# Kernel optimization log

Hardware: AMD Instinct MI355X
Metric: run time of the kernel (lower is better)

Reference implementation:

```python
import jax, jax.numpy as jnp
import numpy as np

D_MODEL = 512
D_STATE = 16
D_CONV = 4
EXPAND = 2
D_INNER = EXPAND * D_MODEL  # 1024
DT_RANK = D_MODEL // 16     # 32 (ceil(512/16))
BATCH, SEQ = 8, 1024


def setup_inputs() -> dict:
    key = jax.random.key(0)
    ks = jax.random.split(key, 10)
    w = lambda i, shape, s=0.02: (jax.random.normal(ks[i], shape, jnp.float32) * s)
    return {
        "x": jax.random.normal(ks[0], (BATCH, SEQ, D_MODEL), jnp.float32),
        # Mamba params
        "W_in": w(1, (2 * D_INNER, D_MODEL)),            # in_proj (no bias)
        "conv_w": w(2, (D_INNER, D_CONV), 0.1),          # depthwise causal conv
        "conv_b": jnp.zeros((D_INNER,), jnp.float32),
        "W_x": w(3, (DT_RANK + 2 * D_STATE, D_INNER)),   # x_proj (no bias)
        "W_dt": w(4, (D_INNER, DT_RANK)),                # dt_proj
        "b_dt": jnp.full((D_INNER,), -4.6, jnp.float32), # -> softplus ~ 0.01
        "A_log": jnp.log(jnp.broadcast_to(
            jnp.arange(1, D_STATE + 1, dtype=jnp.float32), (D_INNER, D_STATE))),
        "D": jnp.ones((D_INNER,), jnp.float32),
        "W_out": w(5, (D_MODEL, D_INNER)),               # out_proj (no bias)
        # LayerNorm + head
        "ln_g": jnp.ones((D_MODEL,), jnp.float32),
        "ln_b": jnp.zeros((D_MODEL,), jnp.float32),
        "head_W": w(6, (D_MODEL, D_MODEL)),
        "head_b": jnp.zeros((D_MODEL,), jnp.float32),
    }


def reference(x, W_in, conv_w, conv_b, W_x, W_dt, b_dt, A_log, D, W_out,
              ln_g, ln_b, head_W, head_b):
    B, L, _ = x.shape
    # in_proj -> split into x branch and gate z
    xz = x @ W_in.T                               # (B, L, 2*D_INNER)
    xi, z = jnp.split(xz, 2, axis=-1)
    # causal depthwise conv1d over time (pad left d_conv-1), then SiLU
    xp = jnp.pad(xi, ((0, 0), (D_CONV - 1, 0), (0, 0)))
    xc = conv_b + sum(conv_w[:, k] * xp[:, k:k + L, :] for k in range(D_CONV))
    xc = jax.nn.silu(xc)                          # (B, L, D_INNER)
    # x_proj -> dt, B, C
    dbc = xc @ W_x.T
    dt = jax.nn.softplus(dbc[..., :DT_RANK] @ W_dt.T + b_dt)   # (B, L, D_INNER)
    Bm = dbc[..., DT_RANK:DT_RANK + D_STATE]                   # (B, L, D_STATE)
    Cm = dbc[..., DT_RANK + D_STATE:]                          # (B, L, D_STATE)
    A = -jnp.exp(A_log)                                        # (D_INNER, D_STATE)

    def step(h, ins):
        dt_t, B_t, C_t, u_t = ins                 # (B,Din) (B,Ds) (B,Ds) (B,Din)
        dA = jnp.exp(dt_t[:, :, None] * A)        # (B, Din, Ds)
        h = dA * h + (dt_t * u_t)[:, :, None] * B_t[:, None, :]
        y = jnp.einsum('bds,bs->bd', h, C_t)
        return h, y

    h0 = jnp.zeros((B, D_INNER, D_STATE), x.dtype)
    xs = (dt.transpose(1, 0, 2), Bm.transpose(1, 0, 2),
          Cm.transpose(1, 0, 2), xc.transpose(1, 0, 2))
    _, ys = jax.lax.scan(step, h0, xs)            # ys: (L, B, D_INNER)
    y = ys.transpose(1, 0, 2) + D * xc
    y = y * jax.nn.silu(z)
    out = y @ W_out.T                             # (B, L, D_MODEL)
    # LayerNorm is per-token, so norm the last token only (== LN(out)[:, -1])
    last = out[:, -1, :]
    mu = last.mean(-1, keepdims=True)
    var = ((last - mu) ** 2).mean(-1, keepdims=True)
    lastn = (last - mu) / jnp.sqrt(var + 1e-5) * ln_g + ln_b
    return lastn @ head_W.T + head_b              # (B, D_MODEL)
```

## Files before the change

kernel.cpp:

```cpp
#include <hip/hip_runtime.h>
#include <stdint.h>

#define B_   8
#define L_   1024
#define DM   512
#define DI   1024
#define DS   16
#define DTR  32
#define M_   (B_*L_)

typedef short v8s __attribute__((ext_vector_type(8)));
typedef short v4s __attribute__((ext_vector_type(4)));
typedef float v4f __attribute__((ext_vector_type(4)));

static __device__ __forceinline__ short f2bf(float f) {
  union { float f; uint32_t u; } v; v.f = f;
  uint32_t r = v.u + 0x7FFFu + ((v.u >> 16) & 1u);
  return (short)(r >> 16);
}
static __device__ __forceinline__ float bf2f(short s) {
  union { uint32_t u; float f; } v; v.u = ((uint32_t)(uint16_t)s) << 16; return v.f;
}
static __device__ __forceinline__ float silu_fast(float a) {
  return a * __builtin_amdgcn_rcpf(1.f + __expf(-a));
}
static __device__ __forceinline__ float wsum(float v) {
#pragma unroll
  for (int o = 32; o > 0; o >>= 1) v += __shfl_xor(v, o, 64);
  return v;
}
static __device__ __forceinline__ void gl_lds16(const short* g, short* l) {
  __builtin_amdgcn_global_load_lds(
      (const __attribute__((address_space(1))) void*)g,
      (__attribute__((address_space(3))) void*)l, 16, 0, 0);
}

__global__ __launch_bounds__(256) void k_prep(const float* __restrict__ x,
                                              const float* __restrict__ w_in,
                                              const float* __restrict__ w_x,
                                              const float* __restrict__ w_dt,
                                              const float* __restrict__ a_log,
                                              short* xb, short* wib, short* wxb, short* wdtb,
                                              float* Aneg, float* zlast) {
  if (blockIdx.x >= 4704) {
    int w = (int)(blockIdx.x - 4704) * 4 + (threadIdx.x >> 6);
    int l = threadIdx.x & 63;
    int b = w >> 10, j = w & 1023;
    const v4f* xr = (const v4f*)(x + ((size_t)(b * L_ + L_ - 1)) * DM);
    const v4f* wr = (const v4f*)(w_in + (size_t)(DI + j) * DM);
    float s = 0.f;
#pragma unroll
    for (int i = 0; i < 2; ++i) {
      v4f a = xr[l + 64 * i], c = wr[l + 64 * i];
      s += a[0]*c[0] + a[1]*c[1] + a[2]*c[2] + a[3]*c[3];
    }
    s = wsum(s);
    if (l == 0) zlast[b * DI + j] = s;
    return;
  }
  int idx = (blockIdx.x * 256 + threadIdx.x) * 4;
  const int n0 = M_ * DM, n1 = DI * DM, n2 = 48 * DI, n3 = DI * DTR, n4 = DI * DS;
  const float* src; short* dst;
  if (idx < n0)              { src = x + idx;    dst = xb + idx; }
  else if ((idx -= n0) < n1) { src = w_in + idx; dst = wib + idx; }
  else if ((idx -= n1) < n2) { src = w_x + idx;  dst = wxb + idx; }
  else if ((idx -= n2) < n3) { src = w_dt + idx; dst = wdtb + idx; }
  else if ((idx -= n3) < n4) {
    v4f v = *(const v4f*)(a_log + idx);
    v4f o;
#pragma unroll
    for (int i = 0; i < 4; ++i) o[i] = -__expf(v[i]);
    *(v4f*)(Aneg + idx) = o;
    return;
  }
  else return;
  v4f v = *(const v4f*)src;
  v4s o;
#pragma unroll
  for (int i = 0; i < 4; ++i) o[i] = f2bf(v[i]);
  *(v4s*)dst = o;
}

__global__ __launch_bounds__(256) void k_gemm_xi(const short* __restrict__ xb,
                                                 const short* __restrict__ wib,
                                                 short* __restrict__ xib) {
  __shared__ short sh[128 * 136];
  short* lA = sh;
  short* lB = sh + 128 * 64;
  int mb = blockIdx.x >> 3, nb = blockIdx.x & 7;
  int tid = threadIdx.x;
  int w = tid >> 6, l = tid & 63, lm = l & 15, q = l >> 4;
  int wm = (w >> 1) * 64, wn = (w & 1) * 64;

  v4f acc[4][4];
#pragma unroll
  for (int i = 0; i < 4; ++i)
#pragma unroll
    for (int j = 0; j < 4; ++j) acc[i][j] = (v4f){0,0,0,0};

  int srow_in_chunk = l >> 3;
  int sslot = l & 7;
  const short* Abase = xb  + (size_t)(mb * 128) * DM;
  const short* Bbase = wib + (size_t)(nb * 128) * DM;

  for (int k0 = 0; k0 < DM; k0 += 64) {
    if (k0) __syncthreads();
#pragma unroll
    for (int i = 0; i < 4; ++i) {
      int chunk = w * 4 + i;
      int row = chunk * 8 + srow_in_chunk;
      int c = sslot ^ (row & 7);
      gl_lds16(Abase + (size_t)row * DM + k0 + c * 8, lA + chunk * 512);
      gl_lds16(Bbase + (size_t)row * DM + k0 + c * 8, lB + chunk * 512);
    }
    __syncthreads();
#pragma unroll
    for (int kt = 0; kt < 2; ++kt) {
      v8s af[4], bf[4];
      int p = (kt * 4 + q) ^ (lm & 7);
#pragma unroll
      for (int t = 0; t < 4; ++t) {
        af[t] = *(const v8s*)(lA + (wm + t * 16 + lm) * 64 + p * 8);
        bf[t] = *(const v8s*)(lB + (wn + t * 16 + lm) * 64 + p * 8);
      }
#pragma unroll
      for (int i = 0; i < 4; ++i)
#pragma unroll
        for (int j = 0; j < 4; ++j)
          acc[i][j] = __builtin_amdgcn_mfma_f32_16x16x32_bf16(af[i], bf[j], acc[i][j], 0, 0, 0);
    }
  }
  __syncthreads();
#pragma unroll
  for (int i = 0; i < 4; ++i)
#pragma unroll
    for (int r = 0; r < 4; ++r) {
      int row = wm + i * 16 + q * 4 + r;
#pragma unroll
      for (int j = 0; j < 4; ++j)
        sh[row * 136 + wn + j * 16 + lm] = f2bf(acc[i][j][r]);
    }
  __syncthreads();
  int cc = tid & 15;
#pragma unroll
  for (int g = 0; g < 8; ++g) {
    int rr = (tid >> 4) + g * 16;
    v8s v = *(const v8s*)(sh + rr * 136 + cc * 8);
    *(v8s*)(xib + (size_t)(mb * 128 + rr) * DI + nb * 128 + cc * 8) = v;
  }
}

__global__ __launch_bounds__(256) void k_conv(const short* __restrict__ xib,
                                              const float* __restrict__ conv_w,
                                              const float* __restrict__ conv_b,
                                              short* __restrict__ xcb,
                                              float* __restrict__ xclast) {
  int bid = blockIdx.x;
  int b = bid >> 7, tc = bid & 127;
  int tid = threadIdx.x;
  int d8 = tid & 127, th = tid >> 7;
  int d = d8 * 8;
  int t0 = tc * 8 + th * 4;
  v4f cw[8];
  float cb[8];
#pragma unroll
  for (int i = 0; i < 8; ++i) {
    cw[i] = *(const v4f*)(conv_w + (d + i) * 4);
    cb[i] = conv_b[d + i];
  }
  float w0[8], w1[8], w2[8];
  const short* base = xib + (size_t)(b * L_) * DI + d;
  short* obase = xcb + (size_t)(b * L_) * DI + d;
#pragma unroll
  for (int i = 0; i < 8; ++i) { w0[i] = 0.f; w1[i] = 0.f; w2[i] = 0.f; }
  if (t0 >= 3) {
    v8s v0 = *(const v8s*)(base + (size_t)(t0 - 3) * DI);
    v8s v1 = *(const v8s*)(base + (size_t)(t0 - 2) * DI);
    v8s v2 = *(const v8s*)(base + (size_t)(t0 - 1) * DI);
#pragma unroll
    for (int i = 0; i < 8; ++i) { w0[i] = bf2f(v0[i]); w1[i] = bf2f(v1[i]); w2[i] = bf2f(v2[i]); }
  }
#pragma unroll
  for (int t = t0; t < t0 + 4; ++t) {
    v8s cur = *(const v8s*)(base + (size_t)t * DI);
    v8s ob;
#pragma unroll
    for (int i = 0; i < 8; ++i) {
      float xv = bf2f(cur[i]);
      float a = cb[i] + cw[i][0] * w0[i] + cw[i][1] * w1[i] + cw[i][2] * w2[i] + cw[i][3] * xv;
      float s = silu_fast(a);
      ob[i] = f2bf(s);
      if (t == L_ - 1) xclast[b * DI + d + i] = s;
      w0[i] = w1[i]; w1[i] = w2[i]; w2[i] = xv;
    }
    *(v8s*)(obase + (size_t)t * DI) = ob;
  }
}

__global__ __launch_bounds__(256) void k_dbcdt(const short* __restrict__ xcb,
                                               const short* __restrict__ wxb,
                                               const short* __restrict__ wdtb,
                                               const float* __restrict__ b_dt,
                                               float* __restrict__ Bmat,
                                               _Float16* __restrict__ dtO,
                                               float* __restrict__ csum2) {
  __shared__ union {
    float red[4 * 16 * 49];
    _Float16 dtile[16 * 1024];
  } u;
  __shared__ short ta[16 * 32];
  int m = blockIdx.x;
  int tid = threadIdx.x, w = tid >> 6, l = tid & 63, lm = l & 15, q = l >> 4;
  v4f a0 = {0,0,0,0}, a1 = {0,0,0,0}, a2 = {0,0,0,0};
  const short* ap = xcb + (size_t)(m * 16 + lm) * DI + w * 256 + q * 8;
  const short* b0 = wxb + (size_t)lm * DI        + w * 256 + q * 8;
  const short* b1 = wxb + (size_t)(16 + lm) * DI + w * 256 + q * 8;
  const short* b2 = wxb + (size_t)(32 + lm) * DI + w * 256 + q * 8;
#pragma unroll
  for (int kk = 0; kk < 8; ++kk) {
    v8s a = *(const v8s*)(ap + kk * 32);
    a0 = __builtin_amdgcn_mfma_f32_16x16x32_bf16(a, *(const v8s*)(b0 + kk * 32), a0, 0, 0, 0);
    a1 = __builtin_amdgcn_mfma_f32_16x16x32_bf16(a, *(const v8s*)(b1 + kk * 32), a1, 0, 0, 0);
    a2 = __builtin_amdgcn_mfma_f32_16x16x32_bf16(a, *(const v8s*)(b2 + kk * 32), a2, 0, 0, 0);
  }
#pragma unroll
  for (int r = 0; r < 4; ++r) {
    int row = q * 4 + r;
    u.red[w * 784 + row * 49 + lm]      = a0[r];
    u.red[w * 784 + row * 49 + 16 + lm] = a1[r];
    u.red[w * 784 + row * 49 + 32 + lm] = a2[r];
  }
  __syncthreads();
  {
    int row = tid >> 4, c0 = tid & 15;
    int base = row * 49 + c0;
    float s0 = u.red[base] + u.red[784 + base] + u.red[1568 + base] + u.red[2352 + base];
    float s1 = u.red[base + 16] + u.red[784 + base + 16] + u.red[1568 + base + 16] + u.red[2352 + base + 16];
    float s2 = u.red[base + 32] + u.red[784 + base + 32] + u.red[1568 + base + 32] + u.red[2352 + base + 32];
    ta[row * 32 + c0]      = f2bf(s0);
    ta[row * 32 + 16 + c0] = f2bf(s1);
    Bmat[(size_t)(m * 16 + row) * DS + c0] = s2;
  }
  __syncthreads();
  v8s ad = *(const v8s*)(ta + lm * 32 + q * 8);
#pragma unroll 4
  for (int nn = 0; nn < 16; ++nn) {
    int nt = w * 16 + nn;
    v8s bb = *(const v8s*)(wdtb + (size_t)(nt * 16 + lm) * DTR + q * 8);
    v4f zz = {0,0,0,0};
    v4f dd = __builtin_amdgcn_mfma_f32_16x16x32_bf16(ad, bb, zz, 0, 0, 0);
    int col = nt * 16 + lm;
    float bd = b_dt[col];
    float s = 0.f;
#pragma unroll
    for (int r = 0; r < 4; ++r) {
      float v = dd[r] + bd;
      float sp = (v > 15.f) ? v : __logf(1.f + __expf(v));
      u.dtile[(q * 4 + r) * 1024 + col] = (_Float16)sp;
      s += sp;
    }
    s += __shfl_xor(s, 16, 64);
    s += __shfl_xor(s, 32, 64);
    if (q == 0) csum2[(size_t)m * DI + col] = s;
  }
  __syncthreads();
#pragma unroll
  for (int row = 0; row < 16; ++row) {
    v4s v = *(const v4s*)(u.dtile + row * 1024 + tid * 4);
    *(v4s*)(dtO + (size_t)(m * 16 + row) * DI + tid * 4) = v;
  }
}

__global__ __launch_bounds__(256) void k_sufc(const float* __restrict__ csum2,
                                              const float* __restrict__ xclast,
                                              const float* __restrict__ w_x,
                                              float* __restrict__ SS,
                                              float* __restrict__ clast) {
  if (blockIdx.x < 32) {
    int b = blockIdx.x >> 2, dseg = blockIdx.x & 3;
    int d = dseg * 256 + threadIdx.x;
    float run = 0.f;
    for (int ch = 31; ch >= 0; --ch) {
      SS[(size_t)(b * 32 + ch) * DI + d] = run;
      run += csum2[(size_t)(b * 64 + 2 * ch + 1) * DI + d]
           + csum2[(size_t)(b * 64 + 2 * ch) * DI + d];
    }
  } else {
    int w2 = (int)(blockIdx.x - 32) * 4 + (threadIdx.x >> 6);
    int l = threadIdx.x & 63;
    int b = w2 >> 4, ss = w2 & 15;
    const v4f* xr = (const v4f*)(xclast + (size_t)b * DI);
    const v4f* wr = (const v4f*)(w_x + (size_t)(48 + ss) * DI);
    float s = 0.f;
#pragma unroll
    for (int i = 0; i < 4; ++i) {
      v4f a = xr[l + 64 * i], c = wr[l + 64 * i];
      s += a[0]*c[0] + a[1]*c[1] + a[2]*c[2] + a[3]*c[3];
    }
    s = wsum(s);
    if (l == 0) clast[b * 16 + ss] = s;
  }
}

__global__ __launch_bounds__(256) void k_scan(const _Float16* __restrict__ dt,
                                              const short* __restrict__ xcb,
                                              const float* __restrict__ Bmat,
                                              const float* __restrict__ SS,
                                              const float* __restrict__ Aneg,
                                              const float* __restrict__ clast,
                                              float* __restrict__ ypart) {
  __shared__ float lB[32 * 16];
  int bid = blockIdx.x;
  int b = bid >> 7, ch = (bid >> 2) & 31, dg = bid & 3;
  int tid = threadIdx.x;
  for (int i = tid; i < 32 * 16; i += 256)
    lB[i] = Bmat[(size_t)(b * L_ + ch * 32) * DS + i];
  __syncthreads();
  int d = dg * 256 + tid;
  float S = SS[(size_t)(b * 32 + ch) * DI + d];
  float As2[16];
#pragma unroll
  for (int s = 0; s < 16; ++s) As2[s] = Aneg[d * 16 + s] * 1.44269504f;
  float h[16];
#pragma unroll
  for (int s = 0; s < 16; ++s) h[s] = 0.f;
  const _Float16* dtp = dt + ((size_t)(b * L_ + ch * 32)) * DI + d;
  const short* xcp = xcb + ((size_t)(b * L_ + ch * 32)) * DI + d;
  for (int tl = 31; tl >= 0; --tl) {
    float dtv = (float)dtp[(size_t)tl * DI];
    float u   = bf2f(xcp[(size_t)tl * DI]);
    float c = dtv * u;
#pragma unroll
    for (int s = 0; s < 16; ++s)
      h[s] += __builtin_amdgcn_exp2f(As2[s] * S) * (c * lB[tl * 16 + s]);
    S += dtv;
  }
  float yp = 0.f;
#pragma unroll
  for (int s = 0; s < 16; ++s) yp += h[s] * clast[b * 16 + s];
  ypart[(size_t)(b * 32 + ch) * DI + d] = yp;
}

__global__ __launch_bounds__(256) void k_ylast(const float* __restrict__ ypart,
                                               const float* __restrict__ xclast,
                                               const float* __restrict__ Dp,
                                               const float* __restrict__ zlast,
                                               float* __restrict__ ylast) {
  int idx = blockIdx.x * 256 + threadIdx.x;
  int b = idx >> 10, d = idx & 1023;
  float acc = 0.f;
#pragma unroll 8
  for (int ch = 0; ch < 32; ++ch) acc += ypart[(size_t)(b * 32 + ch) * DI + d];
  float y = acc + Dp[d] * xclast[idx];
  ylast[idx] = y * silu_fast(zlast[idx]);
}

__global__ __launch_bounds__(256) void k_out(const float* __restrict__ ylast,
                                             const float* __restrict__ w_out,
                                             float* __restrict__ olast) {
  int w = blockIdx.x * 4 + (threadIdx.x >> 6);
  int l = threadIdx.x & 63;
  int b = w >> 9, i = w & 511;
  const v4f* yr = (const v4f*)(ylast + (size_t)b * DI);
  const v4f* wr = (const v4f*)(w_out + (size_t)i * DI);
  float s = 0.f;
#pragma unroll
  for (int k = 0; k < 4; ++k) {
    v4f a = yr[l + 64 * k], c = wr[l + 64 * k];
    s += a[0]*c[0] + a[1]*c[1] + a[2]*c[2] + a[3]*c[3];
  }
  s = wsum(s);
  if (l == 0) olast[b * DM + i] = s;
}

__global__ __launch_bounds__(256) void k_ln(const float* __restrict__ olast,
                                            const float* __restrict__ g,
                                            const float* __restrict__ be,
                                            float* __restrict__ lastn) {
  __shared__ float s1[256], s2[256];
  int b = blockIdx.x, tid = threadIdx.x;
  float v0 = olast[b * DM + tid], v1 = olast[b * DM + 256 + tid];
  s1[tid] = v0 + v1; s2[tid] = v0 * v0 + v1 * v1;
  __syncthreads();
  for (int o = 128; o > 0; o >>= 1) {
    if (tid < o) { s1[tid] += s1[tid + o]; s2[tid] += s2[tid + o]; }
    __syncthreads();
  }
  float mu = s1[0] / (float)DM;
  float var = s2[0] / (float)DM - mu * mu;
  float inv = 1.f / sqrtf(var + 1e-5f);
  lastn[b * DM + tid]       = (v0 - mu) * inv * g[tid]       + be[tid];
  lastn[b * DM + 256 + tid] = (v1 - mu) * inv * g[tid + 256] + be[tid + 256];
}

__global__ __launch_bounds__(256) void k_head(const float* __restrict__ lastn,
                                              const float* __restrict__ hw,
                                              const float* __restrict__ hb,
                                              float* __restrict__ out) {
  int w = blockIdx.x * 4 + (threadIdx.x >> 6);
  int l = threadIdx.x & 63;
  int b = w >> 9, o = w & 511;
  const v4f* xr = (const v4f*)(lastn + (size_t)b * DM);
  const v4f* wr = (const v4f*)(hw + (size_t)o * DM);
  float s = 0.f;
#pragma unroll
  for (int k = 0; k < 2; ++k) {
    v4f a = xr[l + 64 * k], c = wr[l + 64 * k];
    s += a[0]*c[0] + a[1]*c[1] + a[2]*c[2] + a[3]*c[3];
  }
  s = wsum(s);
  if (l == 0) out[b * DM + o] = s + hb[o];
}

extern "C" void kernel_launch(void* const* d_in, const int* in_sizes, int n_in,
                              void* d_out, int out_size, void* d_ws, size_t ws_size,
                              hipStream_t stream) {
  const float* x      = (const float*)d_in[0];
  const float* w_in   = (const float*)d_in[1];
  const float* conv_w = (const float*)d_in[2];
  const float* conv_b = (const float*)d_in[3];
  const float* w_x    = (const float*)d_in[4];
  const float* w_dt   = (const float*)d_in[5];
  const float* b_dt   = (const float*)d_in[6];
  const float* a_log  = (const float*)d_in[7];
  const float* Dp     = (const float*)d_in[8];
  const float* w_out  = (const float*)d_in[9];
  const float* ln_g   = (const float*)d_in[10];
  const float* ln_b   = (const float*)d_in[11];
  const float* head_W = (const float*)d_in[12];
  const float* head_b = (const float*)d_in[13];
  float* out = (float*)d_out;

  char* ws = (char*)d_ws;
  size_t off = 0;
  auto alloc = [&](size_t bytes) { void* p = ws + off; off += (bytes + 255) & ~(size_t)255; return p; };
  short* xb     = (short*)alloc((size_t)M_*DM*2);
  short* wib    = (short*)alloc((size_t)DI*DM*2);
  short* wxb    = (short*)alloc((size_t)48*DI*2);
  short* wdtb   = (short*)alloc((size_t)DI*DTR*2);
  float* Aneg   = (float*)alloc((size_t)DI*DS*4);
  short* xib    = (short*)alloc((size_t)M_*DI*2);
  short* xcb    = (short*)alloc((size_t)M_*DI*2);
  _Float16* dt  = (_Float16*)alloc((size_t)M_*DI*2);
  float* Bmat   = (float*)alloc((size_t)M_*DS*4);
  float* csum2  = (float*)alloc((size_t)512*DI*4);
  float* SS     = (float*)alloc((size_t)B_*32*DI*4);
  float* ypart  = (float*)alloc((size_t)B_*32*DI*4);
  float* zlast  = (float*)alloc((size_t)B_*DI*4);
  float* clast  = (float*)alloc((size_t)B_*DS*4);
  float* xclast = (float*)alloc((size_t)B_*DI*4);
  float* ylast  = (float*)alloc((size_t)B_*DI*4);
  float* olast  = (float*)alloc((size_t)B_*DM*4);
  float* lastn  = (float*)alloc((size_t)B_*DM*4);

  k_prep<<<6752, 256, 0, stream>>>(x, w_in, w_x, w_dt, a_log, xb, wib, wxb, wdtb, Aneg, zlast);
  k_gemm_xi<<<512, 256, 0, stream>>>(xb, wib, xib);
  k_conv<<<1024, 256, 0, stream>>>(xib, conv_w, conv_b, xcb, xclast);
  k_dbcdt<<<512, 256, 0, stream>>>(xcb, wxb, wdtb, b_dt, Bmat, dt, csum2);
  k_sufc<<<64, 256, 0, stream>>>(csum2, xclast, w_x, SS, clast);
  k_scan<<<1024, 256, 0, stream>>>(dt, xcb, Bmat, SS, Aneg, clast, ypart);
  k_ylast<<<32, 256, 0, stream>>>(ypart, xclast, Dp, zlast, ylast);
  k_out<<<1024, 256, 0, stream>>>(ylast, w_out, olast);
  k_ln<<<8, 256, 0, stream>>>(olast, ln_g, ln_b, lastn);
  k_head<<<1024, 256, 0, stream>>>(lastn, head_W, head_b, out);
}
```

Measured before the change: 180.2 us.

## Fuse causal depthwise conv and SiLU into the in_proj GEMM epilogue

```diff
diff --git a/kernel.cpp b/kernel.cpp
--- a/kernel.cpp
+++ b/kernel.cpp
@@ -81,10 +81,14 @@
   *(v4s*)dst = o;
 }
 
-__global__ __launch_bounds__(256) void k_gemm_xi(const short* __restrict__ xb,
-                                                 const short* __restrict__ wib,
-                                                 short* __restrict__ xib) {
+__global__ __launch_bounds__(256) void k_gemm_xi_conv(const short* __restrict__ xb,
+                                                      const short* __restrict__ wib,
+                                                      const float* __restrict__ conv_w,
+                                                      const float* __restrict__ conv_b,
+                                                      short* __restrict__ xcb,
+                                                      float* __restrict__ xclast) {
   __shared__ short sh[128 * 136];
+  __shared__ short hs[3 * 128];
   short* lA = sh;
   short* lB = sh + 128 * 64;
   int mb = blockIdx.x >> 3, nb = blockIdx.x & 7;
@@ -140,60 +144,66 @@
       for (int j = 0; j < 4; ++j)
         sh[row * 136 + wn + j * 16 + lm] = f2bf(acc[i][j][r]);
     }
-  __syncthreads();
-  int cc = tid & 15;
-#pragma unroll
-  for (int g = 0; g < 8; ++g) {
-    int rr = (tid >> 4) + g * 16;
-    v8s v = *(const v8s*)(sh + rr * 136 + cc * 8);
-    *(v8s*)(xib + (size_t)(mb * 128 + rr) * DI + nb * 128 + cc * 8) = v;
-  }
-}
-
-__global__ __launch_bounds__(256) void k_conv(const short* __restrict__ xib,
-                                              const float* __restrict__ conv_w,
-                                              const float* __restrict__ conv_b,
-                                              short* __restrict__ xcb,
-                                              float* __restrict__ xclast) {
-  int bid = blockIdx.x;
-  int b = bid >> 7, tc = bid & 127;
-  int tid = threadIdx.x;
-  int d8 = tid & 127, th = tid >> 7;
-  int d = d8 * 8;
-  int t0 = tc * 8 + th * 4;
-  v4f cw[8];
-  float cb[8];
-#pragma unroll
-  for (int i = 0; i < 8; ++i) {
-    cw[i] = *(const v4f*)(conv_w + (d + i) * 4);
-    cb[i] = conv_b[d + i];
-  }
-  float w0[8], w1[8], w2[8];
-  const short* base = xib + (size_t)(b * L_) * DI + d;
-  short* obase = xcb + (size_t)(b * L_) * DI + d;
-#pragma unroll
-  for (int i = 0; i < 8; ++i) { w0[i] = 0.f; w1[i] = 0.f; w2[i] = 0.f; }
-  if (t0 >= 3) {
-    v8s v0 = *(const v8s*)(base + (size_t)(t0 - 3) * DI);
-    v8s v1 = *(const v8s*)(base + (size_t)(t0 - 2) * DI);
-    v8s v2 = *(const v8s*)(base + (size_t)(t0 - 1) * DI);
-#pragma unroll
-    for (int i = 0; i < 8; ++i) { w0[i] = bf2f(v0[i]); w1[i] = bf2f(v1[i]); w2[i] = bf2f(v2[i]); }
-  }
-#pragma unroll
-  for (int t = t0; t < t0 + 4; ++t) {
-    v8s cur = *(const v8s*)(base + (size_t)t * DI);
-    v8s ob;
-#pragma unroll
-    for (int i = 0; i < 8; ++i) {
-      float xv = bf2f(cur[i]);
-      float a = cb[i] + cw[i][0] * w0[i] + cw[i][1] * w1[i] + cw[i][2] * w2[i] + cw[i][3] * xv;
+  {
+    int t0 = (mb & 7) * 128;
+    int c = tid & 127;
+    if (t0 == 0) {
+      if (tid < 128) { hs[c] = 0; hs[128 + c] = 0; }
+      else           { hs[256 + c] = 0; }
+    } else {
+      const short* wrow = wib + (size_t)(nb * 128 + c) * DM;
+      if (tid < 128) {
+        const short* a0p = xb + (size_t)(mb * 128 - 3) * DM;
+        const short* a1p = xb + (size_t)(mb * 128 - 2) * DM;
+        float s0 = 0.f, s1 = 0.f;
+        for (int k = 0; k < DM; k += 8) {
+          v8s wv  = *(const v8s*)(wrow + k);
+          v8s av0 = *(const v8s*)(a0p + k);
+          v8s av1 = *(const v8s*)(a1p + k);
+#pragma unroll
+          for (int i = 0; i < 8; ++i) {
+            float wf = bf2f(wv[i]);
+            s0 += bf2f(av0[i]) * wf;
+            s1 += bf2f(av1[i]) * wf;
+          }
+        }
+        hs[c] = f2bf(s0); hs[128 + c] = f2bf(s1);
+      } else {
+        const short* a2p = xb + (size_t)(mb * 128 - 1) * DM;
+        float s2 = 0.f;
+        for (int k = 0; k < DM; k += 8) {
+          v8s wv  = *(const v8s*)(wrow + k);
+          v8s av2 = *(const v8s*)(a2p + k);
+#pragma unroll
+          for (int i = 0; i < 8; ++i) s2 += bf2f(av2[i]) * bf2f(wv[i]);
+        }
+        hs[256 + c] = f2bf(s2);
+      }
+    }
+  }
+  __syncthreads();
+  {
+    int c = tid & 127, th = tid >> 7;
+    int gcol = nb * 128 + c;
+    v4f cw = *(const v4f*)(conv_w + gcol * 4);
+    float cb = conv_b[gcol];
+    float w0, w1, w2;
+    if (th == 0) {
+      w0 = bf2f(hs[c]); w1 = bf2f(hs[128 + c]); w2 = bf2f(hs[256 + c]);
+    } else {
+      w0 = bf2f(sh[61 * 136 + c]); w1 = bf2f(sh[62 * 136 + c]); w2 = bf2f(sh[63 * 136 + c]);
+    }
+    size_t outbase = (size_t)(mb * 128 + th * 64) * DI + gcol;
+    bool lastblk = ((mb & 7) == 7) && (th == 1);
+    int b = mb >> 3;
+    for (int r = 0; r < 64; ++r) {
+      float xv = bf2f(sh[(th * 64 + r) * 136 + c]);
+      float a = cb + cw[0] * w0 + cw[1] * w1 + cw[2] * w2 + cw[3] * xv;
       float s = silu_fast(a);
-      ob[i] = f2bf(s);
-      if (t == L_ - 1) xclast[b * DI + d + i] = s;
-      w0[i] = w1[i]; w1[i] = w2[i]; w2[i] = xv;
-    }
-    *(v8s*)(obase + (size_t)t * DI) = ob;
+      xcb[outbase + (size_t)r * DI] = f2bf(s);
+      if (lastblk && r == 63) xclast[b * DI + gcol] = s;
+      w0 = w1; w1 = w2; w2 = xv;
+    }
   }
 }
 
@@ -439,7 +449,6 @@
   short* wxb    = (short*)alloc((size_t)48*DI*2);
   short* wdtb   = (short*)alloc((size_t)DI*DTR*2);
   float* Aneg   = (float*)alloc((size_t)DI*DS*4);
-  short* xib    = (short*)alloc((size_t)M_*DI*2);
   short* xcb    = (short*)alloc((size_t)M_*DI*2);
   _Float16* dt  = (_Float16*)alloc((size_t)M_*DI*2);
   float* Bmat   = (float*)alloc((size_t)M_*DS*4);
@@ -454,8 +463,7 @@
   float* lastn  = (float*)alloc((size_t)B_*DM*4);
 
   k_prep<<<6752, 256, 0, stream>>>(x, w_in, w_x, w_dt, a_log, xb, wib, wxb, wdtb, Aneg, zlast);
-  k_gemm_xi<<<512, 256, 0, stream>>>(xb, wib, xib);
-  k_conv<<<1024, 256, 0, stream>>>(xib, conv_w, conv_b, xcb, xclast);
+  k_gemm_xi_conv<<<512, 256, 0, stream>>>(xb, wib, conv_w, conv_b, xcb, xclast);
   k_dbcdt<<<512, 256, 0, stream>>>(xcb, wxb, wdtb, b_dt, Bmat, dt, csum2);
   k_sufc<<<64, 256, 0, stream>>>(csum2, xclast, w_x, SS, clast);
   k_scan<<<1024, 256, 0, stream>>>(dt, xcb, Bmat, SS, Aneg, clast, ypart);
```

Result: slower. 193.5 us (+7.4%).
